# Kernel tuning notes

Hardware: AMD Instinct MI355X
Metric: run time of the kernel (lower is better)

The kernel has to match this reference:

```python
import jax, jax.numpy as jnp
import numpy as np

N_NODES = 30000
N_EDGES = 480000
N_REL = 16
DIM = 128
N_TRIPLES = 200000


def _xavier(key, shape):
    fan_in, fan_out = shape[-2], shape[-1]
    limit = np.sqrt(6.0 / (fan_in + fan_out)).astype(np.float32)
    return jax.random.uniform(key, shape, jnp.float32, -limit, limit)


def setup_inputs() -> dict:
    key = jax.random.key(0)
    ks = jax.random.split(key, 12)
    inp = {
        "node_emb": _xavier(ks[0], (N_NODES, DIM)),
        "rel_emb": _xavier(ks[1], (N_REL, DIM)),
        "W_rel0": _xavier(ks[2], (N_REL, DIM, DIM)),
        "Wself_w0": _xavier(ks[3], (DIM, DIM)),
        "Wself_b0": jnp.zeros((DIM,), jnp.float32),
        "W_rel1": _xavier(ks[4], (N_REL, DIM, DIM)),
        "Wself_w1": _xavier(ks[5], (DIM, DIM)),
        "Wself_b1": jnp.zeros((DIM,), jnp.float32),
        "local_nodes": jnp.arange(N_NODES, dtype=jnp.int32),
        "edge_index": jax.random.randint(ks[6], (2, N_EDGES), 0, N_NODES, jnp.int32),
        "edge_type": jax.random.randint(ks[7], (N_EDGES,), 0, N_REL, jnp.int32),
        "h_loc": jax.random.randint(ks[8], (N_TRIPLES,), 0, N_NODES, jnp.int32),
        "r_ids": jax.random.randint(ks[9], (N_TRIPLES,), 0, N_REL, jnp.int32),
        "t_loc": jax.random.randint(ks[10], (N_TRIPLES,), 0, N_NODES, jnp.int32),
    }
    return inp


def _rgcn_layer(x, edge_index, edge_type, W_rel, Ww, Wb):
    # x: [N, in], W_rel: [R, in, out], Ww: [out, in] (torch Linear layout)
    N = x.shape[0]
    out = x @ Ww.T + Wb                                 # self loop [N, out]
    src, dst = edge_index[0], edge_index[1]
    # transform every node under every relation, then gather per edge:
    # math-equivalent to bmm(x[src][:,None,:], W_rel[rel]) in the original,
    # but avoids materializing [E, in, out].
    xt = jnp.einsum('ni,rio->rno', x, W_rel)            # [R, N, out]
    msg = xt[edge_type, src]                            # [E, out]
    agg = jax.ops.segment_sum(msg, dst, num_segments=N)  # [N, out]
    deg = jax.ops.segment_sum(jnp.ones(dst.shape, x.dtype), dst, num_segments=N)
    deg = jnp.maximum(deg, 1.0)[:, None]
    return jax.nn.relu(out + agg / deg)


def reference(node_emb, rel_emb, W_rel0, Wself_w0, Wself_b0,
              W_rel1, Wself_w1, Wself_b1,
              local_nodes, edge_index, edge_type, h_loc, r_ids, t_loc):
    x = node_emb[local_nodes]                           # [N, d]
    x = _rgcn_layer(x, edge_index, edge_type, W_rel0, Wself_w0, Wself_b0)
    x = _rgcn_layer(x, edge_index, edge_type, W_rel1, Wself_w1, Wself_b1)
    # DistMult scoring on local embeddings
    scores = jnp.sum(x[h_loc] * rel_emb[r_ids] * x[t_loc], axis=-1)  # [B]
    return scores
```

## Files before the change

### kernel.cpp

```cpp
#include <hip/hip_runtime.h>

#define NN 30000
#define NE 480000
#define NR 16
#define D  128
#define NT 200000
#define AST 132
#define NBLK 235
#define NBINS (NBLK * NR)


__global__ void k_gather_x(const float* __restrict__ node_emb,
                           const int* __restrict__ local_nodes,
                           float* __restrict__ x) {
  int i4 = blockIdx.x * blockDim.x + threadIdx.x;
  if (i4 >= NN * (D / 4)) return;
  int n = i4 >> 5, c = i4 & 31;
  int src = local_nodes[n];
  reinterpret_cast<float4*>(x)[i4] =
      reinterpret_cast<const float4*>(node_emb)[(size_t)src * 32 + c];
}

__global__ void k_hist_bins(const int* __restrict__ ei, const int* __restrict__ et,
                            int* __restrict__ bins) {
  int e = blockIdx.x * blockDim.x + threadIdx.x;
  if (e >= NE) return;
  int d = ei[NE + e], r = et[e];
  atomicAdd(&bins[(d >> 7) * NR + r], 1);
}

__global__ void k_scan_bins(const int* __restrict__ bins, int* __restrict__ off,
                            int* __restrict__ cur) {
  __shared__ int ps[1024];
  const int t = threadIdx.x;
  const int base = t * 4;
  int c[4], s0 = 0;
#pragma unroll
  for (int u = 0; u < 4; ++u) {
    int b = base + u;
    c[u] = (b < NBINS) ? bins[b] : 0;
    s0 += c[u];
  }
  ps[t] = s0;
  __syncthreads();
  for (int dstep = 1; dstep < 1024; dstep <<= 1) {
    int v = (t >= dstep) ? ps[t - dstep] : 0;
    __syncthreads();
    ps[t] += v;
    __syncthreads();
  }
  int ex = ps[t] - s0;
#pragma unroll
  for (int u = 0; u < 4; ++u) {
    int b = base + u;
    if (b <= NBINS) {
      off[b] = ex;
      if (b < NBINS) cur[b] = ex;
    }
    ex += c[u];
  }
}

__global__ void k_fill(const int* __restrict__ ei, const int* __restrict__ et,
                       int* __restrict__ cur, int* __restrict__ srt,
                       float* __restrict__ deg) {
  int e = blockIdx.x * blockDim.x + threadIdx.x;
  if (e >= NE) return;
  int s = ei[e], d = ei[NE + e], r = et[e];
  int p = atomicAdd(&cur[(d >> 7) * NR + r], 1);
  srt[p] = ((d & 127) << 16) | s;
  atomicAdd(&deg[d], 1.0f);
}

__global__ void k_transposeW(const float* __restrict__ W0, const float* __restrict__ W1,
                             float* __restrict__ T0, float* __restrict__ T1) {
  const float* W = blockIdx.x ? W1 : W0;
  float* T = blockIdx.x ? T1 : T0;
  for (int idx = threadIdx.x; idx < D * D; idx += 256) {
    int o = idx >> 7, k = idx & 127;
    T[k * D + o] = W[idx];
  }
}


__launch_bounds__(256, 1)
__global__ void k_fused(const float* __restrict__ x, const float* __restrict__ Wrel,
                        const float* __restrict__ WT, const float* __restrict__ Wb,
                        const int* __restrict__ srt, const int* __restrict__ off,
                        const float* __restrict__ deg, float* __restrict__ xo) {
  __shared__ float S[D][AST];
  __shared__ float Wl[D][D];
  const int nb = blockIdx.x;
  const int row0 = nb * D;
  const int tx = threadIdx.x & 15, ty = threadIdx.x >> 4;
  const int wave = threadIdx.x >> 6, lane = threadIdx.x & 63;

  float acc[8][8];
#pragma unroll
  for (int j = 0; j < 8; ++j)
#pragma unroll
    for (int m = 0; m < 8; ++m) acc[j][m] = 0.f;

  for (int r = 0; r < NR; ++r) {
    __syncthreads();
#pragma unroll
    for (int t = 0; t < 17; ++t) {
      int idx = threadIdx.x + 256 * t;
      if (idx < D * AST / 4)
        reinterpret_cast<float4*>(&S[0][0])[idx] = make_float4(0.f, 0.f, 0.f, 0.f);
    }
    __syncthreads();
    {
      const float4* Wr4 = reinterpret_cast<const float4*>(Wrel + (size_t)r * D * D);
      float4* Wl4 = reinterpret_cast<float4*>(&Wl[0][0]);
#pragma unroll
      for (int t = 0; t < 16; ++t)
        Wl4[threadIdx.x + 256 * t] = Wr4[threadIdx.x + 256 * t];
    }
    {
      const int b = nb * NR + r;
      const int end = off[b + 1];
      int i = off[b] + wave;
      int pv_n = 0;
      float2 v_n = make_float2(0.f, 0.f);
      if (i < end) {
        pv_n = srt[i];
        v_n = reinterpret_cast<const float2*>(x + (size_t)(pv_n & 0xFFFF) * D)[lane];
      }
      for (; i < end; i += 4) {
        const int pv_c = pv_n;
        const float2 v_c = v_n;
        const int i2 = i + 4;
        if (i2 < end) {
          pv_n = srt[i2];
          v_n = reinterpret_cast<const float2*>(x + (size_t)(pv_n & 0xFFFF) * D)[lane];
        }
        const int dl = pv_c >> 16;
        atomicAdd(&S[dl][2 * lane], v_c.x);
        atomicAdd(&S[dl][2 * lane + 1], v_c.y);
      }
    }
    __syncthreads();
    for (int k = 0; k < D; k += 4) {
      float4 a[8];
#pragma unroll
      for (int j = 0; j < 8; ++j)
        a[j] = *reinterpret_cast<const float4*>(&S[ty + 16 * j][k]);
#pragma unroll
      for (int kk = 0; kk < 4; ++kk) {
        float4 w0 = *reinterpret_cast<const float4*>(&Wl[k + kk][4 * tx]);
        float4 w1 = *reinterpret_cast<const float4*>(&Wl[k + kk][4 * tx + 64]);
#pragma unroll
        for (int j = 0; j < 8; ++j) {
          float av = (kk == 0) ? a[j].x : (kk == 1) ? a[j].y
                   : (kk == 2) ? a[j].z : a[j].w;
          acc[j][0] += av * w0.x; acc[j][1] += av * w0.y;
          acc[j][2] += av * w0.z; acc[j][3] += av * w0.w;
          acc[j][4] += av * w1.x; acc[j][5] += av * w1.y;
          acc[j][6] += av * w1.z; acc[j][7] += av * w1.w;
        }
      }
    }
  }

#pragma unroll
  for (int j = 0; j < 8; ++j) {
    int row = row0 + ty + 16 * j;
    float dv = (row < NN) ? deg[row] : 1.f;
    float inv = 1.f / fmaxf(dv, 1.f);
#pragma unroll
    for (int m = 0; m < 8; ++m) acc[j][m] *= inv;
  }

  __syncthreads();
  {
    const float4* WT4 = reinterpret_cast<const float4*>(WT);
    float4* Wl4 = reinterpret_cast<float4*>(&Wl[0][0]);
#pragma unroll
    for (int t = 0; t < 16; ++t)
      Wl4[threadIdx.x + 256 * t] = WT4[threadIdx.x + 256 * t];
#pragma unroll
    for (int t = 0; t < 16; ++t) {
      int idx = threadIdx.x + 256 * t;
      int rw = idx >> 5, c = idx & 31;
      float4 v = make_float4(0.f, 0.f, 0.f, 0.f);
      if (row0 + rw < NN)
        v = reinterpret_cast<const float4*>(x)[(size_t)(row0 + rw) * 32 + c];
      *reinterpret_cast<float4*>(&S[rw][4 * c]) = v;
    }
  }
  __syncthreads();
  for (int k = 0; k < D; k += 4) {
    float4 a[8];
#pragma unroll
    for (int j = 0; j < 8; ++j)
      a[j] = *reinterpret_cast<const float4*>(&S[ty + 16 * j][k]);
#pragma unroll
    for (int kk = 0; kk < 4; ++kk) {
      float4 w0 = *reinterpret_cast<const float4*>(&Wl[k + kk][4 * tx]);
      float4 w1 = *reinterpret_cast<const float4*>(&Wl[k + kk][4 * tx + 64]);
#pragma unroll
      for (int j = 0; j < 8; ++j) {
        float av = (kk == 0) ? a[j].x : (kk == 1) ? a[j].y
                 : (kk == 2) ? a[j].z : a[j].w;
        acc[j][0] += av * w0.x; acc[j][1] += av * w0.y;
        acc[j][2] += av * w0.z; acc[j][3] += av * w0.w;
        acc[j][4] += av * w1.x; acc[j][5] += av * w1.y;
        acc[j][6] += av * w1.z; acc[j][7] += av * w1.w;
      }
    }
  }

  const float4 b0 = reinterpret_cast<const float4*>(Wb)[tx];
  const float4 b1 = reinterpret_cast<const float4*>(Wb)[tx + 16];
#pragma unroll
  for (int j = 0; j < 8; ++j) {
    int row = row0 + ty + 16 * j;
    if (row < NN) {
      float4 o0, o1;
      o0.x = fmaxf(acc[j][0] + b0.x, 0.f);
      o0.y = fmaxf(acc[j][1] + b0.y, 0.f);
      o0.z = fmaxf(acc[j][2] + b0.z, 0.f);
      o0.w = fmaxf(acc[j][3] + b0.w, 0.f);
      o1.x = fmaxf(acc[j][4] + b1.x, 0.f);
      o1.y = fmaxf(acc[j][5] + b1.y, 0.f);
      o1.z = fmaxf(acc[j][6] + b1.z, 0.f);
      o1.w = fmaxf(acc[j][7] + b1.w, 0.f);
      reinterpret_cast<float4*>(xo + (size_t)row * D)[tx] = o0;
      reinterpret_cast<float4*>(xo + (size_t)row * D)[tx + 16] = o1;
    }
  }
}


__global__ void k_score(const float* __restrict__ x, const float* __restrict__ rel,
                        const int* __restrict__ hh, const int* __restrict__ rr,
                        const int* __restrict__ tt, float* __restrict__ out) {
  int gw = (blockIdx.x * blockDim.x + threadIdx.x) >> 6;
  int lane = threadIdx.x & 63;
  int nw = (gridDim.x * blockDim.x) >> 6;
  for (int i = gw; i < NT; i += nw) {
    const float2* ph = reinterpret_cast<const float2*>(x + (size_t)hh[i] * D);
    const float2* pr = reinterpret_cast<const float2*>(rel + (size_t)rr[i] * D);
    const float2* pt = reinterpret_cast<const float2*>(x + (size_t)tt[i] * D);
    float2 a = ph[lane], b = pr[lane], c = pt[lane];
    float v = a.x * b.x * c.x + a.y * b.y * c.y;
#pragma unroll
    for (int m = 32; m; m >>= 1) v += __shfl_xor(v, m);
    if (lane == 0) out[i] = v;
  }
}


extern "C" void kernel_launch(void* const* d_in, const int* in_sizes, int n_in,
                              void* d_out, int out_size, void* d_ws, size_t ws_size,
                              hipStream_t stream) {
  const float* node_emb = (const float*)d_in[0];
  const float* rel_emb  = (const float*)d_in[1];
  const float* W_rel0   = (const float*)d_in[2];
  const float* Wself_w0 = (const float*)d_in[3];
  const float* Wself_b0 = (const float*)d_in[4];
  const float* W_rel1   = (const float*)d_in[5];
  const float* Wself_w1 = (const float*)d_in[6];
  const float* Wself_b1 = (const float*)d_in[7];
  const int* local_nodes = (const int*)d_in[8];
  const int* edge_index  = (const int*)d_in[9];
  const int* edge_type   = (const int*)d_in[10];
  const int* h_loc = (const int*)d_in[11];
  const int* r_ids = (const int*)d_in[12];
  const int* t_loc = (const int*)d_in[13];
  float* out = (float*)d_out;

  char* ws = (char*)d_ws;
  float* x_a = (float*)(ws + 0);
  float* x_b = (float*)(ws + 15360000);
  float* WT0 = (float*)(ws + 30720000);
  float* WT1 = (float*)(ws + 30785536);
  float* deg = (float*)(ws + 30851072);
  int* bins  = (int*)(ws + 30971072);
  int* off   = (int*)(ws + 30986112);
  int* cur   = (int*)(ws + 31001156);
  int* srt   = (int*)(ws + 31016196);
  if (ws_size < (size_t)32936196) return;

  hipMemsetAsync(ws + 30851072, 0, 135040, stream);

  k_gather_x<<<3750, 256, 0, stream>>>(node_emb, local_nodes, x_a);
  k_hist_bins<<<1875, 256, 0, stream>>>(edge_index, edge_type, bins);
  k_scan_bins<<<1, 1024, 0, stream>>>(bins, off, cur);
  k_fill<<<1875, 256, 0, stream>>>(edge_index, edge_type, cur, srt, deg);
  k_transposeW<<<2, 256, 0, stream>>>(Wself_w0, Wself_w1, WT0, WT1);

  k_fused<<<NBLK, 256, 0, stream>>>(x_a, W_rel0, WT0, Wself_b0, srt, off, deg, x_b);
  k_fused<<<NBLK, 256, 0, stream>>>(x_b, W_rel1, WT1, Wself_b1, srt, off, deg, x_a);

  k_score<<<1024, 256, 0, stream>>>(x_a, rel_emb, h_loc, r_ids, t_loc, out);
}
```

Measured before the change: 1.431 ms.

## Overlap next-relation edge gather with GEMM and read weights from global

Restructures the fused RGCN layer kernel so the edge gathers for relation r+1 are issued into registers (up to 16 per wave) before the relation-r GEMM runs. The deposit into shared memory happens after the GEMM, so gather latency is hidden behind compute. The block grows to 512 threads with a 4-column-per-thread tile, and the shared-memory weight staging is removed: weights are read straight from global memory through the cache. This saves LDS space and copy work, but makes the GEMM's inner loop depend on global/L1 load latency and raises register pressure from the prefetch buffers.

Measured after the change: 1.479 ms. +3.3%, slower.

```diff
diff --git a/kernel.cpp b/kernel.cpp
--- a/kernel.cpp
+++ b/kernel.cpp
@@ -8,6 +8,7 @@
 #define AST 132
 #define NBLK 235
 #define NBINS (NBLK * NR)
+#define PF 16
 
 
 __global__ void k_gather_x(const float* __restrict__ node_emb,
@@ -83,84 +84,105 @@
 }
 
 
-__launch_bounds__(256, 1)
+__device__ __forceinline__ void gemm_tile(const float (*S)[AST],
+                                          const float* __restrict__ Wg,
+                                          int tx, int ty, float acc[8][4]) {
+  const float4* __restrict__ W4 = reinterpret_cast<const float4*>(Wg);
+#pragma unroll 8
+  for (int k = 0; k < D; k += 4) {
+    float4 a[8];
+#pragma unroll
+    for (int j = 0; j < 8; ++j)
+      a[j] = *reinterpret_cast<const float4*>(&S[ty + 16 * j][k]);
+    float4 w[4];
+#pragma unroll
+    for (int kk = 0; kk < 4; ++kk) w[kk] = W4[(k + kk) * 32 + tx];
+#pragma unroll
+    for (int kk = 0; kk < 4; ++kk) {
+#pragma unroll
+      for (int j = 0; j < 8; ++j) {
+        float av = (kk == 0) ? a[j].x : (kk == 1) ? a[j].y
+                 : (kk == 2) ? a[j].z : a[j].w;
+        acc[j][0] += av * w[kk].x;
+        acc[j][1] += av * w[kk].y;
+        acc[j][2] += av * w[kk].z;
+        acc[j][3] += av * w[kk].w;
+      }
+    }
+  }
+}
+
+__launch_bounds__(512, 2)
 __global__ void k_fused(const float* __restrict__ x, const float* __restrict__ Wrel,
                         const float* __restrict__ WT, const float* __restrict__ Wb,
                         const int* __restrict__ srt, const int* __restrict__ off,
                         const float* __restrict__ deg, float* __restrict__ xo) {
   __shared__ float S[D][AST];
-  __shared__ float Wl[D][D];
   const int nb = blockIdx.x;
   const int row0 = nb * D;
-  const int tx = threadIdx.x & 15, ty = threadIdx.x >> 4;
+  const int tx = threadIdx.x & 31, ty = threadIdx.x >> 5;
   const int wave = threadIdx.x >> 6, lane = threadIdx.x & 63;
-
-  float acc[8][8];
+  const float2* __restrict__ x2 = reinterpret_cast<const float2*>(x);
+
+  float acc[8][4];
 #pragma unroll
   for (int j = 0; j < 8; ++j)
 #pragma unroll
-    for (int m = 0; m < 8; ++m) acc[j][m] = 0.f;
+    for (int m = 0; m < 4; ++m) acc[j][m] = 0.f;
+
+  int pv[PF];
+  float2 pvv[PF];
+
+  auto zeroS = [&]() {
+    float4* S4 = reinterpret_cast<float4*>(&S[0][0]);
+#pragma unroll
+    for (int t = 0; t < 9; ++t) {
+      int idx = threadIdx.x + 512 * t;
+      if (idx < D * AST / 4) S4[idx] = make_float4(0.f, 0.f, 0.f, 0.f);
+    }
+  };
+  auto loadE = [&](int b) {
+    const int base = off[b], end = off[b + 1];
+#pragma unroll
+    for (int t = 0; t < PF; ++t) {
+      int i = base + wave + 8 * t;
+      pv[t] = (i < end) ? srt[i] : -1;
+    }
+#pragma unroll
+    for (int t = 0; t < PF; ++t)
+      pvv[t] = (pv[t] >= 0) ? x2[(size_t)(pv[t] & 0xFFFF) * 64 + lane]
+                            : make_float2(0.f, 0.f);
+  };
+  auto depositE = [&](int b) {
+#pragma unroll
+    for (int t = 0; t < PF; ++t)
+      if (pv[t] >= 0) {
+        int dl = pv[t] >> 16;
+        atomicAdd(&S[dl][2 * lane], pvv[t].x);
+        atomicAdd(&S[dl][2 * lane + 1], pvv[t].y);
+      }
+    const int end = off[b + 1];
+    for (int i = off[b] + 8 * PF + wave; i < end; i += 8) {
+      int p = srt[i];
+      float2 vv = x2[(size_t)(p & 0xFFFF) * 64 + lane];
+      atomicAdd(&S[p >> 16][2 * lane], vv.x);
+      atomicAdd(&S[p >> 16][2 * lane + 1], vv.y);
+    }
+  };
+
+  zeroS();
+  __syncthreads();
+  loadE(nb * NR);
+  depositE(nb * NR);
 
   for (int r = 0; r < NR; ++r) {
     __syncthreads();
-#pragma unroll
-    for (int t = 0; t < 17; ++t) {
-      int idx = threadIdx.x + 256 * t;
-      if (idx < D * AST / 4)
-        reinterpret_cast<float4*>(&S[0][0])[idx] = make_float4(0.f, 0.f, 0.f, 0.f);
-    }
-    __syncthreads();
-    {
-      const float4* Wr4 = reinterpret_cast<const float4*>(Wrel + (size_t)r * D * D);
-      float4* Wl4 = reinterpret_cast<float4*>(&Wl[0][0]);
-#pragma unroll
-      for (int t = 0; t < 16; ++t)
-        Wl4[threadIdx.x + 256 * t] = Wr4[threadIdx.x + 256 * t];
-    }
-    {
-      const int b = nb * NR + r;
-      const int end = off[b + 1];
-      int i = off[b] + wave;
-      int pv_n = 0;
-      float2 v_n = make_float2(0.f, 0.f);
-      if (i < end) {
-        pv_n = srt[i];
-        v_n = reinterpret_cast<const float2*>(x + (size_t)(pv_n & 0xFFFF) * D)[lane];
-      }
-      for (; i < end; i += 4) {
-        const int pv_c = pv_n;
-        const float2 v_c = v_n;
-        const int i2 = i + 4;
-        if (i2 < end) {
-          pv_n = srt[i2];
-          v_n = reinterpret_cast<const float2*>(x + (size_t)(pv_n & 0xFFFF) * D)[lane];
-        }
-        const int dl = pv_c >> 16;
-        atomicAdd(&S[dl][2 * lane], v_c.x);
-        atomicAdd(&S[dl][2 * lane + 1], v_c.y);
-      }
-    }
-    __syncthreads();
-    for (int k = 0; k < D; k += 4) {
-      float4 a[8];
-#pragma unroll
-      for (int j = 0; j < 8; ++j)
-        a[j] = *reinterpret_cast<const float4*>(&S[ty + 16 * j][k]);
-#pragma unroll
-      for (int kk = 0; kk < 4; ++kk) {
-        float4 w0 = *reinterpret_cast<const float4*>(&Wl[k + kk][4 * tx]);
-        float4 w1 = *reinterpret_cast<const float4*>(&Wl[k + kk][4 * tx + 64]);
-#pragma unroll
-        for (int j = 0; j < 8; ++j) {
-          float av = (kk == 0) ? a[j].x : (kk == 1) ? a[j].y
-                   : (kk == 2) ? a[j].z : a[j].w;
-          acc[j][0] += av * w0.x; acc[j][1] += av * w0.y;
-          acc[j][2] += av * w0.z; acc[j][3] += av * w0.w;
-          acc[j][4] += av * w1.x; acc[j][5] += av * w1.y;
-          acc[j][6] += av * w1.z; acc[j][7] += av * w1.w;
-        }
-      }
-    }
+    if (r + 1 < NR) loadE(nb * NR + r + 1);
+    gemm_tile(S, Wrel + (size_t)r * D * D, tx, ty, acc);
+    __syncthreads();
+    zeroS();
+    __syncthreads();
+    if (r + 1 < NR) depositE(nb * NR + r + 1);
   }
 
 #pragma unroll
@@ -169,65 +191,32 @@
     float dv = (row < NN) ? deg[row] : 1.f;
     float inv = 1.f / fmaxf(dv, 1.f);
 #pragma unroll
-    for (int m = 0; m < 8; ++m) acc[j][m] *= inv;
-  }
-
+    for (int m = 0; m < 4; ++m) acc[j][m] *= inv;
+  }
+
+#pragma unroll
+  for (int t = 0; t < 8; ++t) {
+    int idx = threadIdx.x + 512 * t;
+    int rw = idx >> 5, c = idx & 31;
+    float4 vv = make_float4(0.f, 0.f, 0.f, 0.f);
+    if (row0 + rw < NN)
+      vv = reinterpret_cast<const float4*>(x)[(size_t)(row0 + rw) * 32 + c];
+    *reinterpret_cast<float4*>(&S[rw][4 * c]) = vv;
+  }
   __syncthreads();
-  {
-    const float4* WT4 = reinterpret_cast<const float4*>(WT);
-    float4* Wl4 = reinterpret_cast<float4*>(&Wl[0][0]);
-#pragma unroll
-    for (int t = 0; t < 16; ++t)
-      Wl4[threadIdx.x + 256 * t] = WT4[threadIdx.x + 256 * t];
-#pragma unroll
-    for (int t = 0; t < 16; ++t) {
-      int idx = threadIdx.x + 256 * t;
-      int rw = idx >> 5, c = idx & 31;
-      float4 v = make_float4(0.f, 0.f, 0.f, 0.f);
-      if (row0 + rw < NN)
-        v = reinterpret_cast<const float4*>(x)[(size_t)(row0 + rw) * 32 + c];
-      *reinterpret_cast<float4*>(&S[rw][4 * c]) = v;
-    }
-  }
-  __syncthreads();
-  for (int k = 0; k < D; k += 4) {
-    float4 a[8];
-#pragma unroll
-    for (int j = 0; j < 8; ++j)
-      a[j] = *reinterpret_cast<const float4*>(&S[ty + 16 * j][k]);
-#pragma unroll
-    for (int kk = 0; kk < 4; ++kk) {
-      float4 w0 = *reinterpret_cast<const float4*>(&Wl[k + kk][4 * tx]);
-      float4 w1 = *reinterpret_cast<const float4*>(&Wl[k + kk][4 * tx + 64]);
-#pragma unroll
-      for (int j = 0; j < 8; ++j) {
-        float av = (kk == 0) ? a[j].x : (kk == 1) ? a[j].y
-                 : (kk == 2) ? a[j].z : a[j].w;
-        acc[j][0] += av * w0.x; acc[j][1] += av * w0.y;
-        acc[j][2] += av * w0.z; acc[j][3] += av * w0.w;
-        acc[j][4] += av * w1.x; acc[j][5] += av * w1.y;
-        acc[j][6] += av * w1.z; acc[j][7] += av * w1.w;
-      }
-    }
-  }
-
-  const float4 b0 = reinterpret_cast<const float4*>(Wb)[tx];
-  const float4 b1 = reinterpret_cast<const float4*>(Wb)[tx + 16];
+  gemm_tile(S, WT, tx, ty, acc);
+
+  const float4 bb = reinterpret_cast<const float4*>(Wb)[tx];
 #pragma unroll
   for (int j = 0; j < 8; ++j) {
     int row = row0 + ty + 16 * j;
     if (row < NN) {
-      float4 o0, o1;
-      o0.x = fmaxf(acc[j][0] + b0.x, 0.f);
-      o0.y = fmaxf(acc[j][1] + b0.y, 0.f);
-      o0.z = fmaxf(acc[j][2] + b0.z, 0.f);
-      o0.w = fmaxf(acc[j][3] + b0.w, 0.f);
-      o1.x = fmaxf(acc[j][4] + b1.x, 0.f);
-      o1.y = fmaxf(acc[j][5] + b1.y, 0.f);
-      o1.z = fmaxf(acc[j][6] + b1.z, 0.f);
-      o1.w = fmaxf(acc[j][7] + b1.w, 0.f);
-      reinterpret_cast<float4*>(xo + (size_t)row * D)[tx] = o0;
-      reinterpret_cast<float4*>(xo + (size_t)row * D)[tx + 16] = o1;
+      float4 o;
+      o.x = fmaxf(acc[j][0] + bb.x, 0.f);
+      o.y = fmaxf(acc[j][1] + bb.y, 0.f);
+      o.z = fmaxf(acc[j][2] + bb.z, 0.f);
+      o.w = fmaxf(acc[j][3] + bb.w, 0.f);
+      reinterpret_cast<float4*>(xo + (size_t)row * D)[tx] = o;
     }
   }
 }
@@ -291,8 +280,8 @@
   k_fill<<<1875, 256, 0, stream>>>(edge_index, edge_type, cur, srt, deg);
   k_transposeW<<<2, 256, 0, stream>>>(Wself_w0, Wself_w1, WT0, WT1);
 
-  k_fused<<<NBLK, 256, 0, stream>>>(x_a, W_rel0, WT0, Wself_b0, srt, off, deg, x_b);
-  k_fused<<<NBLK, 256, 0, stream>>>(x_b, W_rel1, WT1, Wself_b1, srt, off, deg, x_a);
+  k_fused<<<NBLK, 512, 0, stream>>>(x_a, W_rel0, WT0, Wself_b0, srt, off, deg, x_b);
+  k_fused<<<NBLK, 512, 0, stream>>>(x_b, W_rel1, WT1, Wself_b1, srt, off, deg, x_a);
 
   k_score<<<1024, 256, 0, stream>>>(x_a, rel_emb, h_loc, r_ids, t_loc, out);
 }
```
